# Kernel tuning notes

Hardware: AMD Instinct MI355X
Metric: run time of the kernel (lower is better)

Reference implementation:

```python
import jax, jax.numpy as jnp
import numpy as np

B, S, D = 4, 2048, 1024


def setup_inputs() -> dict:
    key = jax.random.key(0)
    ks = jax.random.split(key, 7)
    s = 1.0 / np.sqrt(D)
    return {
        "x": jax.random.normal(ks[0], (B, S, D), dtype=jnp.float32),
        "Wq": jax.random.normal(ks[1], (D, D), dtype=jnp.float32) * s,
        "bq": jnp.zeros((D,), dtype=jnp.float32),
        "Wk": jax.random.normal(ks[2], (D, D), dtype=jnp.float32) * s,
        "bk": jnp.zeros((D,), dtype=jnp.float32),
        "Wv": jax.random.normal(ks[3], (D, D), dtype=jnp.float32) * s,
        "bv": jnp.zeros((D,), dtype=jnp.float32),
    }


def reference(x, Wq, bq, Wk, bk, Wv, bv):
    # Linear layers: x @ W^T + b (torch nn.Linear convention)
    Q = jnp.einsum("bsd,ed->bse", x, Wq) + bq
    K = jnp.einsum("bsd,ed->bse", x, Wk) + bk
    V = jnp.einsum("bsd,ed->bse", x, Wv) + bv
    scale = 1.0 / (x.shape[-1] ** 0.5)
    scores = jnp.einsum("bse,bte->bst", Q, K) * scale  # [B, S, S]
    attn = jax.nn.softmax(scores, axis=-1)
    out = jnp.einsum("bst,bte->bse", attn, V)
    return out
```

## Files before the change

kernel.cpp:

```cpp
#include <hip/hip_runtime.h>
#include <math.h>


typedef _Float16 f16;
typedef _Float16 f16x8 __attribute__((ext_vector_type(8)));
typedef _Float16 f16x4 __attribute__((ext_vector_type(4)));
typedef float f32x4 __attribute__((ext_vector_type(4)));

__device__ __forceinline__ void glds16(const void* g, const void* l) {
    __builtin_amdgcn_global_load_lds(
        (const __attribute__((address_space(1))) void*)g,
        (__attribute__((address_space(3))) void*)l, 16, 0, 0);
}

__global__ __launch_bounds__(256) void cvt16_kernel(
    const float* __restrict__ in, f16* __restrict__ o, int n4)
{
    int i = blockIdx.x * 256 + threadIdx.x;
    if (i >= n4) return;
    float4 v = ((const float4*)in)[i];
    f16x4 h = { (f16)v.x, (f16)v.y, (f16)v.z, (f16)v.w };
    ((f16x4*)o)[i] = h;
}

__global__ __launch_bounds__(256) void cvtw_kernel(
    const float* __restrict__ Wq, const float* __restrict__ Wk,
    const float* __restrict__ Wv, f16* __restrict__ o, int n4)
{
    int i = blockIdx.x * 256 + threadIdx.x;
    if (i >= n4) return;
    const float* src = (blockIdx.y == 0) ? Wq : (blockIdx.y == 1) ? Wk : Wv;
    float4 v = ((const float4*)src)[i];
    f16x4 h = { (f16)v.x, (f16)v.y, (f16)v.z, (f16)v.w };
    ((f16x4*)(o + (size_t)blockIdx.y * 1024 * 1024))[i] = h;
}

__global__ __launch_bounds__(256) void zero_kernel(float* __restrict__ p, int n)
{
    int i = blockIdx.x * 256 + threadIdx.x;
    if (i < n) p[i] = 0.0f;
}

__device__ __forceinline__ void mfma_core1(
    const f16* __restrict__ A, int lda,
    const f16* __restrict__ B, int ldb,
    int K, int m0, int n0, f16* sm, f32x4 acc[4][4])
{
    f16* sA = sm;
    f16* sB = sm + 4096;

    const int tid  = threadIdx.x;
    const int lane = tid & 63;
    const int wave = tid >> 6;
    const int wm = (wave >> 1) * 64;
    const int wn = (wave & 1) * 64;
    const int lr = lane & 15;
    const int kq = lane >> 4;

    const int srow = wave * 32;
    const int grow = srow + (lane >> 2);
    const int gcol = (lane & 3) * 8;

    const f16* gA = A + (size_t)(m0 + grow) * lda + gcol;
    const f16* gB = B + (size_t)(n0 + grow) * ldb + gcol;
    const size_t rsA = (size_t)16 * lda;
    const size_t rsB = (size_t)16 * ldb;

    f16* lA = sA + srow * 32;
    f16* lB = sB + srow * 32;

    for (int k0 = 0; k0 < K; k0 += 32) {
        glds16(gA + k0,       lA);
        glds16(gA + k0 + rsA, lA + 512);
        glds16(gB + k0,       lB);
        glds16(gB + k0 + rsB, lB + 512);
        __syncthreads();

        f16x8 a[4], b[4];
        #pragma unroll
        for (int i = 0; i < 4; ++i) {
            a[i] = *(const f16x8*)&sA[(wm + i * 16 + lr) * 32 + kq * 8];
            b[i] = *(const f16x8*)&sB[(wn + i * 16 + lr) * 32 + kq * 8];
        }
        #pragma unroll
        for (int i = 0; i < 4; ++i)
            #pragma unroll
            for (int j = 0; j < 4; ++j)
                acc[i][j] = __builtin_amdgcn_mfma_f32_16x16x32_f16(a[i], b[j], acc[i][j], 0, 0, 0);
        __syncthreads();
    }
}

__global__ __launch_bounds__(256) void qkv_mfma_kernel(
    const f16* __restrict__ xh, const f16* __restrict__ Wh,
    const float* __restrict__ bq, const float* __restrict__ bk,
    const float* __restrict__ bv,
    f16* __restrict__ Qh, f16* __restrict__ Kh, f16* __restrict__ Vt)
{
    __shared__ __align__(16) f16 smem[8448];
    const int z  = blockIdx.z;
    const int m0 = blockIdx.y * 128;
    const int n0 = blockIdx.x * 128;

    f32x4 acc[4][4];
    #pragma unroll
    for (int i = 0; i < 4; ++i)
        #pragma unroll
        for (int j = 0; j < 4; ++j) acc[i][j] = (f32x4){0.f, 0.f, 0.f, 0.f};

    mfma_core1(xh, 1024, Wh + (size_t)z * 1024 * 1024, 1024, 1024, m0, n0, smem, acc);

    const int tid  = threadIdx.x;
    const int lane = tid & 63;
    const int wave = tid >> 6;
    const int wm = (wave >> 1) * 64;
    const int wn = (wave & 1) * 64;
    const int col  = lane & 15;
    const int quad = lane >> 4;

    if (z == 2) {
        const int b    = m0 >> 11;
        const int tloc = m0 & 2047;
        #pragma unroll
        for (int p = 0; p < 2; ++p) {
            if ((wave >> 1) == p) {
                #pragma unroll
                for (int j = 0; j < 4; ++j) {
                    const int cl = wn + j * 16 + col;
                    const float bb = bv[n0 + cl];
                    #pragma unroll
                    for (int i = 0; i < 4; ++i)
                        #pragma unroll
                        for (int r = 0; r < 4; ++r) {
                            const int rl = i * 16 + quad * 4 + r;
                            smem[rl * 132 + cl] = (f16)(acc[i][j][r] + bb);
                        }
                }
            }
            __syncthreads();
            const int dl = tid >> 1;
            const int sb = (tid & 1) * 32;
            f16 buf[32];
            #pragma unroll
            for (int u = 0; u < 32; ++u) buf[u] = smem[(sb + u) * 132 + dl];
            f16* dst = Vt + ((size_t)b * 1024 + n0 + dl) * 2048 + tloc + p * 64 + sb;
            *(f16x8*)(dst)      = *(f16x8*)&buf[0];
            *(f16x8*)(dst + 8)  = *(f16x8*)&buf[8];
            *(f16x8*)(dst + 16) = *(f16x8*)&buf[16];
            *(f16x8*)(dst + 24) = *(f16x8*)&buf[24];
            __syncthreads();
        }
    } else {
        const float* bias = (z == 0) ? bq : bk;
        const float  sc   = (z == 0) ? 0.03125f : 1.0f;
        f16* C = (z == 0) ? Qh : Kh;
        #pragma unroll
        for (int j = 0; j < 4; ++j) {
            const int gn = n0 + wn + j * 16 + col;
            const float bb = bias[gn];
            #pragma unroll
            for (int i = 0; i < 4; ++i)
                #pragma unroll
                for (int r = 0; r < 4; ++r) {
                    const int gm = m0 + wm + i * 16 + quad * 4 + r;
                    C[(size_t)gm * 1024 + gn] = (f16)((acc[i][j][r] + bb) * sc);
                }
        }
    }
}

__global__ __launch_bounds__(256) void scores_exp_kernel(
    const f16* __restrict__ Qh, const f16* __restrict__ Kh,
    f16* __restrict__ P, float* __restrict__ sums, int r0, int R)
{
    __shared__ __align__(16) f16 smem[8192];
    const int b  = blockIdx.z;
    const int m0 = blockIdx.y * 128;
    const int n0 = blockIdx.x * 128;

    f32x4 acc[4][4];
    #pragma unroll
    for (int i = 0; i < 4; ++i)
        #pragma unroll
        for (int j = 0; j < 4; ++j) acc[i][j] = (f32x4){0.f, 0.f, 0.f, 0.f};

    const size_t ao = ((size_t)b * 2048 + r0) * 1024;
    const size_t bo = (size_t)b * 2048 * 1024;
    mfma_core1(Qh + ao, 1024, Kh + bo, 1024, 1024, m0, n0, smem, acc);

    const int lane = threadIdx.x & 63;
    const int wave = threadIdx.x >> 6;
    const int wm = (wave >> 1) * 64;
    const int wn = (wave & 1) * 64;
    const int col  = lane & 15;
    const int quad = lane >> 4;
    f16* C = P + (size_t)b * R * 2048;

    float rp[4][4];
    #pragma unroll
    for (int i = 0; i < 4; ++i)
        #pragma unroll
        for (int r = 0; r < 4; ++r) rp[i][r] = 0.0f;

    #pragma unroll
    for (int i = 0; i < 4; ++i)
        #pragma unroll
        for (int r = 0; r < 4; ++r) {
            const int gm = m0 + wm + i * 16 + quad * 4 + r;
            #pragma unroll
            for (int j = 0; j < 4; ++j) {
                const int gn = n0 + wn + j * 16 + col;
                const f16 p = (f16)__expf(acc[i][j][r]);
                C[(size_t)gm * 2048 + gn] = p;
                rp[i][r] += (float)p;
            }
        }

    #pragma unroll
    for (int i = 0; i < 4; ++i)
        #pragma unroll
        for (int r = 0; r < 4; ++r) {
            float v = rp[i][r];
            v += __shfl_xor(v, 1);
            v += __shfl_xor(v, 2);
            v += __shfl_xor(v, 4);
            v += __shfl_xor(v, 8);
            rp[i][r] = v;
        }
    if (col == 0) {
        #pragma unroll
        for (int i = 0; i < 4; ++i)
            #pragma unroll
            for (int r = 0; r < 4; ++r) {
                const int row = m0 + wm + i * 16 + quad * 4 + r;
                atomicAdd(&sums[b * R + row], rp[i][r]);
            }
    }
}

__global__ __launch_bounds__(256) void pv_mfma_kernel(
    const f16* __restrict__ P, const f16* __restrict__ Vt,
    const float* __restrict__ sums, float* __restrict__ out, int r0, int R)
{
    __shared__ __align__(16) f16 smem[8192];
    const int b  = blockIdx.z;
    const int m0 = blockIdx.y * 128;
    const int n0 = blockIdx.x * 128;

    f32x4 acc[4][4];
    #pragma unroll
    for (int i = 0; i < 4; ++i)
        #pragma unroll
        for (int j = 0; j < 4; ++j) acc[i][j] = (f32x4){0.f, 0.f, 0.f, 0.f};

    const size_t ao = (size_t)b * R * 2048;
    const size_t bo = (size_t)b * 1024 * 2048;
    mfma_core1(P + ao, 2048, Vt + bo, 2048, 2048, m0, n0, smem, acc);

    const int lane = threadIdx.x & 63;
    const int wave = threadIdx.x >> 6;
    const int wm = (wave >> 1) * 64;
    const int wn = (wave & 1) * 64;
    const int col  = lane & 15;
    const int quad = lane >> 4;
    float* C = out + ((size_t)b * 2048 + r0) * 1024;

    #pragma unroll
    for (int i = 0; i < 4; ++i)
        #pragma unroll
        for (int r = 0; r < 4; ++r) {
            const int rl = m0 + wm + i * 16 + quad * 4 + r;
            const float inv = 1.0f / sums[b * R + rl];
            #pragma unroll
            for (int j = 0; j < 4; ++j) {
                const int gn = n0 + wn + j * 16 + col;
                C[(size_t)rl * 1024 + gn] = acc[i][j][r] * inv;
            }
        }
}

extern "C" void kernel_launch(void* const* d_in, const int* in_sizes, int n_in,
                              void* d_out, int out_size, void* d_ws, size_t ws_size,
                              hipStream_t stream)
{
    (void)in_sizes; (void)n_in; (void)out_size;
    const int Bn = 4, S = 2048, D = 1024;
    const float* x  = (const float*)d_in[0];
    const float* Wq = (const float*)d_in[1];
    const float* bq = (const float*)d_in[2];
    const float* Wk = (const float*)d_in[3];
    const float* bk = (const float*)d_in[4];
    const float* Wv = (const float*)d_in[5];
    const float* bv = (const float*)d_in[6];
    float* out = (float*)d_out;

    const size_t MB = 1024 * 1024;
    char* w = (char*)d_ws;
    f16*   xh   = (f16*)(w + 0 * MB);
    f16*   Wh3  = (f16*)(w + 16 * MB);
    f16*   Qh   = (f16*)(w + 22 * MB);
    f16*   Kh   = (f16*)(w + 38 * MB);
    f16*   Vt   = (f16*)(w + 54 * MB);
    float* sums = (float*)(w + 70 * MB);
    f16*   Pexp;

    int R;
    if (ws_size >= 104 * MB) { R = 2048; Pexp = (f16*)(w + 71 * MB); }
    else                     { R = 1024; Pexp = (f16*)(w + 0 * MB);  }

    cvt16_kernel<<<dim3(Bn * S * D / 4 / 256), 256, 0, stream>>>(x, xh, Bn * S * D / 4);
    cvtw_kernel<<<dim3(D * D / 4 / 256, 3), 256, 0, stream>>>(Wq, Wk, Wv, Wh3, D * D / 4);

    qkv_mfma_kernel<<<dim3(D / 128, (Bn * S) / 128, 3), 256, 0, stream>>>(
        xh, Wh3, bq, bk, bv, Qh, Kh, Vt);

    for (int r0 = 0; r0 < S; r0 += R) {
        zero_kernel<<<dim3((Bn * R + 255) / 256), 256, 0, stream>>>(sums, Bn * R);
        scores_exp_kernel<<<dim3(S / 128, R / 128, Bn), 256, 0, stream>>>(
            Qh, Kh, Pexp, sums, r0, R);
        pv_mfma_kernel<<<dim3(D / 128, R / 128, Bn), 256, 0, stream>>>(
            Pexp, Vt, sums, out, r0, R);
    }
}
```

Before: 303.5 us.

## Double GEMM K-tile to 64 with XOR-swizzled LDS and separate V transpose

The shared MFMA GEMM core now stages 64-wide K tiles instead of 32, with an XOR swizzle on the LDS layout to avoid bank conflicts. This halves the number of barrier pairs per GEMM at the cost of twice the LDS per block. The in-kernel V transpose in the QKV projection is replaced by a plain row-major store plus a separate transpose kernel, which adds a launch and an extra pass over V. The workspace layout shifts to fit the new V buffer, and a smaller R fallback is added for tight workspaces.

```diff
diff --git a/kernel.cpp b/kernel.cpp
--- a/kernel.cpp
+++ b/kernel.cpp
@@ -41,13 +41,13 @@
     if (i < n) p[i] = 0.0f;
 }
 
-__device__ __forceinline__ void mfma_core1(
+__device__ __forceinline__ void mfma_core(
     const f16* __restrict__ A, int lda,
     const f16* __restrict__ B, int ldb,
     int K, int m0, int n0, f16* sm, f32x4 acc[4][4])
 {
     f16* sA = sm;
-    f16* sB = sm + 4096;
+    f16* sB = sm + 8192;
 
     const int tid  = threadIdx.x;
     const int lane = tid & 63;
@@ -57,36 +57,42 @@
     const int lr = lane & 15;
     const int kq = lane >> 4;
 
-    const int srow = wave * 32;
-    const int grow = srow + (lane >> 2);
-    const int gcol = (lane & 3) * 8;
-
-    const f16* gA = A + (size_t)(m0 + grow) * lda + gcol;
-    const f16* gB = B + (size_t)(n0 + grow) * ldb + gcol;
-    const size_t rsA = (size_t)16 * lda;
-    const size_t rsB = (size_t)16 * ldb;
-
-    f16* lA = sA + srow * 32;
-    f16* lB = sB + srow * 32;
-
-    for (int k0 = 0; k0 < K; k0 += 32) {
-        glds16(gA + k0,       lA);
-        glds16(gA + k0 + rsA, lA + 512);
-        glds16(gB + k0,       lB);
-        glds16(gB + k0 + rsB, lB + 512);
+    const int srow  = wave * 32;
+    const int rloc  = lane >> 3;
+    const int chunk = (lane & 7) ^ rloc;
+    const int gcol  = chunk * 8;
+
+    const f16* gA = A + (size_t)(m0 + srow + rloc) * lda + gcol;
+    const f16* gB = B + (size_t)(n0 + srow + rloc) * ldb + gcol;
+
+    f16* lA = sA + srow * 64;
+    f16* lB = sB + srow * 64;
+
+    for (int k0 = 0; k0 < K; k0 += 64) {
+        #pragma unroll
+        for (int p = 0; p < 4; ++p) {
+            glds16(gA + k0 + (size_t)(p * 8) * lda, lA + p * 512);
+            glds16(gB + k0 + (size_t)(p * 8) * ldb, lB + p * 512);
+        }
         __syncthreads();
 
-        f16x8 a[4], b[4];
-        #pragma unroll
-        for (int i = 0; i < 4; ++i) {
-            a[i] = *(const f16x8*)&sA[(wm + i * 16 + lr) * 32 + kq * 8];
-            b[i] = *(const f16x8*)&sB[(wn + i * 16 + lr) * 32 + kq * 8];
-        }
-        #pragma unroll
-        for (int i = 0; i < 4; ++i)
-            #pragma unroll
-            for (int j = 0; j < 4; ++j)
-                acc[i][j] = __builtin_amdgcn_mfma_f32_16x16x32_f16(a[i], b[j], acc[i][j], 0, 0, 0);
+        #pragma unroll
+        for (int kk = 0; kk < 2; ++kk) {
+            f16x8 a[4], b[4];
+            #pragma unroll
+            for (int i = 0; i < 4; ++i) {
+                const int ra = wm + i * 16 + lr;
+                const int rb = wn + i * 16 + lr;
+                const int c  = kk * 4 + kq;
+                a[i] = *(const f16x8*)&sA[ra * 64 + ((c ^ (ra & 7)) * 8)];
+                b[i] = *(const f16x8*)&sB[rb * 64 + ((c ^ (rb & 7)) * 8)];
+            }
+            #pragma unroll
+            for (int i = 0; i < 4; ++i)
+                #pragma unroll
+                for (int j = 0; j < 4; ++j)
+                    acc[i][j] = __builtin_amdgcn_mfma_f32_16x16x32_f16(a[i], b[j], acc[i][j], 0, 0, 0);
+        }
         __syncthreads();
     }
 }
@@ -95,9 +101,9 @@
     const f16* __restrict__ xh, const f16* __restrict__ Wh,
     const float* __restrict__ bq, const float* __restrict__ bk,
     const float* __restrict__ bv,
-    f16* __restrict__ Qh, f16* __restrict__ Kh, f16* __restrict__ Vt)
-{
-    __shared__ __align__(16) f16 smem[8448];
+    f16* __restrict__ Qh, f16* __restrict__ Kh, f16* __restrict__ Vh)
+{
+    __shared__ __align__(16) f16 smem[16384];
     const int z  = blockIdx.z;
     const int m0 = blockIdx.y * 128;
     const int n0 = blockIdx.x * 128;
@@ -108,72 +114,63 @@
         #pragma unroll
         for (int j = 0; j < 4; ++j) acc[i][j] = (f32x4){0.f, 0.f, 0.f, 0.f};
 
-    mfma_core1(xh, 1024, Wh + (size_t)z * 1024 * 1024, 1024, 1024, m0, n0, smem, acc);
-
-    const int tid  = threadIdx.x;
-    const int lane = tid & 63;
-    const int wave = tid >> 6;
+    mfma_core(xh, 1024, Wh + (size_t)z * 1024 * 1024, 1024, 1024, m0, n0, smem, acc);
+
+    const float* bias = (z == 0) ? bq : (z == 1) ? bk : bv;
+    const float  sc   = (z == 0) ? 0.03125f : 1.0f;
+    f16* C = (z == 0) ? Qh : (z == 1) ? Kh : Vh;
+    const int lane = threadIdx.x & 63;
+    const int wave = threadIdx.x >> 6;
     const int wm = (wave >> 1) * 64;
     const int wn = (wave & 1) * 64;
     const int col  = lane & 15;
     const int quad = lane >> 4;
 
-    if (z == 2) {
-        const int b    = m0 >> 11;
-        const int tloc = m0 & 2047;
-        #pragma unroll
-        for (int p = 0; p < 2; ++p) {
-            if ((wave >> 1) == p) {
-                #pragma unroll
-                for (int j = 0; j < 4; ++j) {
-                    const int cl = wn + j * 16 + col;
-                    const float bb = bv[n0 + cl];
-                    #pragma unroll
-                    for (int i = 0; i < 4; ++i)
-                        #pragma unroll
-                        for (int r = 0; r < 4; ++r) {
-                            const int rl = i * 16 + quad * 4 + r;
-                            smem[rl * 132 + cl] = (f16)(acc[i][j][r] + bb);
-                        }
-                }
-            }
-            __syncthreads();
-            const int dl = tid >> 1;
-            const int sb = (tid & 1) * 32;
-            f16 buf[32];
-            #pragma unroll
-            for (int u = 0; u < 32; ++u) buf[u] = smem[(sb + u) * 132 + dl];
-            f16* dst = Vt + ((size_t)b * 1024 + n0 + dl) * 2048 + tloc + p * 64 + sb;
-            *(f16x8*)(dst)      = *(f16x8*)&buf[0];
-            *(f16x8*)(dst + 8)  = *(f16x8*)&buf[8];
-            *(f16x8*)(dst + 16) = *(f16x8*)&buf[16];
-            *(f16x8*)(dst + 24) = *(f16x8*)&buf[24];
-            __syncthreads();
-        }
-    } else {
-        const float* bias = (z == 0) ? bq : bk;
-        const float  sc   = (z == 0) ? 0.03125f : 1.0f;
-        f16* C = (z == 0) ? Qh : Kh;
-        #pragma unroll
-        for (int j = 0; j < 4; ++j) {
-            const int gn = n0 + wn + j * 16 + col;
-            const float bb = bias[gn];
-            #pragma unroll
-            for (int i = 0; i < 4; ++i)
-                #pragma unroll
-                for (int r = 0; r < 4; ++r) {
-                    const int gm = m0 + wm + i * 16 + quad * 4 + r;
-                    C[(size_t)gm * 1024 + gn] = (f16)((acc[i][j][r] + bb) * sc);
-                }
-        }
+    #pragma unroll
+    for (int j = 0; j < 4; ++j) {
+        const int gn = n0 + wn + j * 16 + col;
+        const float bb = bias[gn];
+        #pragma unroll
+        for (int i = 0; i < 4; ++i)
+            #pragma unroll
+            for (int r = 0; r < 4; ++r) {
+                const int gm = m0 + wm + i * 16 + quad * 4 + r;
+                C[(size_t)gm * 1024 + gn] = (f16)((acc[i][j][r] + bb) * sc);
+            }
     }
+}
+
+__global__ __launch_bounds__(256) void vtrans_kernel(
+    const f16* __restrict__ V, f16* __restrict__ Vt)
+{
+    __shared__ f16 t[64][72];
+    const int b  = blockIdx.z;
+    const int s0 = blockIdx.x * 64;
+    const int d0 = blockIdx.y * 64;
+    const int tid = threadIdx.x;
+
+    const int r  = tid >> 3;
+    const int c8 = (tid & 7) * 8;
+    const f16* src = V + ((size_t)b * 2048 + s0) * 1024 + d0;
+    *(f16x8*)&t[r][c8]      = *(const f16x8*)(src + (size_t)r * 1024 + c8);
+    *(f16x8*)&t[r + 32][c8] = *(const f16x8*)(src + (size_t)(r + 32) * 1024 + c8);
+    __syncthreads();
+
+    const int dl  = tid >> 2;
+    const int sl0 = (tid & 3) * 16;
+    f16* dst = Vt + ((size_t)b * 1024 + d0 + dl) * 2048 + s0 + sl0;
+    f16 buf[16];
+    #pragma unroll
+    for (int u = 0; u < 16; ++u) buf[u] = t[sl0 + u][dl];
+    *(f16x8*)dst       = *(f16x8*)&buf[0];
+    *(f16x8*)(dst + 8) = *(f16x8*)&buf[8];
 }
 
 __global__ __launch_bounds__(256) void scores_exp_kernel(
     const f16* __restrict__ Qh, const f16* __restrict__ Kh,
     f16* __restrict__ P, float* __restrict__ sums, int r0, int R)
 {
-    __shared__ __align__(16) f16 smem[8192];
+    __shared__ __align__(16) f16 smem[16384];
     const int b  = blockIdx.z;
     const int m0 = blockIdx.y * 128;
     const int n0 = blockIdx.x * 128;
@@ -186,7 +183,7 @@
 
     const size_t ao = ((size_t)b * 2048 + r0) * 1024;
     const size_t bo = (size_t)b * 2048 * 1024;
-    mfma_core1(Qh + ao, 1024, Kh + bo, 1024, 1024, m0, n0, smem, acc);
+    mfma_core(Qh + ao, 1024, Kh + bo, 1024, 1024, m0, n0, smem, acc);
 
     const int lane = threadIdx.x & 63;
     const int wave = threadIdx.x >> 6;
@@ -242,7 +239,7 @@
     const f16* __restrict__ P, const f16* __restrict__ Vt,
     const float* __restrict__ sums, float* __restrict__ out, int r0, int R)
 {
-    __shared__ __align__(16) f16 smem[8192];
+    __shared__ __align__(16) f16 smem[16384];
     const int b  = blockIdx.z;
     const int m0 = blockIdx.y * 128;
     const int n0 = blockIdx.x * 128;
@@ -255,7 +252,7 @@
 
     const size_t ao = (size_t)b * R * 2048;
     const size_t bo = (size_t)b * 1024 * 2048;
-    mfma_core1(P + ao, 2048, Vt + bo, 2048, 2048, m0, n0, smem, acc);
+    mfma_core(P + ao, 2048, Vt + bo, 2048, 2048, m0, n0, smem, acc);
 
     const int lane = threadIdx.x & 63;
     const int wave = threadIdx.x >> 6;
@@ -300,19 +297,22 @@
     f16*   Wh3  = (f16*)(w + 16 * MB);
     f16*   Qh   = (f16*)(w + 22 * MB);
     f16*   Kh   = (f16*)(w + 38 * MB);
-    f16*   Vt   = (f16*)(w + 54 * MB);
-    float* sums = (float*)(w + 70 * MB);
+    f16*   Vh   = (f16*)(w + 54 * MB);
+    f16*   Vt   = (f16*)(w + 70 * MB);
+    float* sums = (float*)(w + 86 * MB);
     f16*   Pexp;
 
     int R;
-    if (ws_size >= 104 * MB) { R = 2048; Pexp = (f16*)(w + 71 * MB); }
-    else                     { R = 1024; Pexp = (f16*)(w + 0 * MB);  }
+    if      (ws_size >= 120 * MB) { R = 2048; Pexp = (f16*)(w + 87 * MB); }
+    else if (ws_size >= 88 * MB)  { R = 1024; Pexp = (f16*)(w + 0 * MB);  }
+    else                          { R = 512;  Pexp = (f16*)(w + 0 * MB);  }
 
     cvt16_kernel<<<dim3(Bn * S * D / 4 / 256), 256, 0, stream>>>(x, xh, Bn * S * D / 4);
     cvtw_kernel<<<dim3(D * D / 4 / 256, 3), 256, 0, stream>>>(Wq, Wk, Wv, Wh3, D * D / 4);
 
     qkv_mfma_kernel<<<dim3(D / 128, (Bn * S) / 128, 3), 256, 0, stream>>>(
-        xh, Wh3, bq, bk, bv, Qh, Kh, Vt);
+        xh, Wh3, bq, bk, bv, Qh, Kh, Vh);
+    vtrans_kernel<<<dim3(S / 64, D / 64, Bn), 256, 0, stream>>>(Vh, Vt);
 
     for (int r0 = 0; r0 < S; r0 += R) {
         zero_kernel<<<dim3((Bn * R + 255) / 256), 256, 0, stream>>>(sums, Bn * R);
```

New measurement: 281.3 us. 1.08x faster.
